# Performance work log

Hardware: AMD Instinct MI355X
Metric: run time of the kernel (lower is better)

Reference implementation:

```python
import jax, jax.numpy as jnp
import numpy as np


def _conv(x, w, stride, padding):
    # x: NCHW, w: OIHW
    return jax.lax.conv_general_dilated(
        x, w,
        window_strides=(stride, stride),
        padding=[(padding, padding), (padding, padding)],
        dimension_numbers=("NCHW", "OIHW", "NCHW"),
    )


def setup_inputs() -> dict:
    key = jax.random.key(0)
    ks = jax.random.split(key, 7)
    N, C_in, H0, W0 = 64, 128, 56, 56
    C_out = 256
    x = jax.random.normal(ks[0], (N, C_in, H0, W0), dtype=jnp.float32)
    w1 = jax.random.normal(ks[1], (C_out, C_in, 3, 3), dtype=jnp.float32) * 0.05
    b1 = jax.random.normal(ks[2], (C_out,), dtype=jnp.float32) * 0.05
    w2 = jax.random.normal(ks[3], (C_out, C_out, 3, 3), dtype=jnp.float32) * 0.05
    b2 = jax.random.normal(ks[4], (C_out,), dtype=jnp.float32) * 0.05
    wds = jax.random.normal(ks[5], (C_out, C_in, 1, 1), dtype=jnp.float32) * 0.05
    bds = jax.random.normal(ks[6], (C_out,), dtype=jnp.float32) * 0.05
    return {"x": x, "w1": w1, "b1": b1, "w2": w2, "b2": b2, "wds": wds, "bds": bds}


def reference(x, w1, b1, w2, b2, wds, bds):
    stride = 2
    # conv1 (BN folded) + bias + ReLU -> act: (N, C_out, H1, W1)
    act = jax.nn.relu(_conv(x, w1, stride, 1) + b1[None, :, None, None])
    # fused: conv2 3x3 (pad 1) + b2 + 1x1 strided downsample of x + bds, then ReLU
    main = _conv(act, w2, 1, 1) + b2[None, :, None, None]
    shortcut = _conv(x, wds, stride, 0) + bds[None, :, None, None]
    return jax.nn.relu(main + shortcut)
```

## Files before the change

kernel.cpp:

```cpp
#include <hip/hip_runtime.h>
#include <hip/hip_bf16.h>

typedef short short8 __attribute__((ext_vector_type(8)));
typedef float floatx4 __attribute__((ext_vector_type(4)));
typedef __hip_bfloat16 bf16;

#define GLB(p) ((const __attribute__((address_space(1))) void*)(p))
#define LDSP(p) ((__attribute__((address_space(3))) void*)(p))

__device__ __forceinline__ void gload16(const bf16* g, char* l) {
    __builtin_amdgcn_global_load_lds(GLB(g), LDSP(l), 16, 0, 0);
}

#define XPAD_BYTES   (64u*58*58*128*2)
#define ACTPAD_BYTES (64u*30*30*256*2)
#define OFF_XPAD   0
#define OFF_ACTPAD (XPAD_BYTES)
#define OFF_W1T    (OFF_ACTPAD + ACTPAD_BYTES)
#define OFF_W2T    (OFF_W1T + 1152u*256*2)
#define OFF_WDST   (OFF_W2T + 2304u*256*2)

__global__ void wtrans_kernel(const float* __restrict__ w1, const float* __restrict__ w2,
                              const float* __restrict__ wds,
                              bf16* __restrict__ w1t, bf16* __restrict__ w2t,
                              bf16* __restrict__ wdst) {
    int i = blockIdx.x * 256 + threadIdx.x;
    if (i < 256 * 1152) {
        int oc = i / 1152, k = i % 1152, tap = k >> 7, ic = k & 127;
        w1t[i] = __float2bfloat16(w1[(oc * 128 + ic) * 9 + tap]);
    }
    if (i < 256 * 2304) {
        int oc = i / 2304, k = i % 2304, tap = k >> 8, ic = k & 255;
        w2t[i] = __float2bfloat16(w2[(oc * 256 + ic) * 9 + tap]);
    }
    if (i < 256 * 128) {
        wdst[i] = __float2bfloat16(wds[i]);
    }
}

__global__ void xpad_kernel(const float* __restrict__ x, bf16* __restrict__ xpad) {
    int bid = blockIdx.x;
    int n = bid / 56, h = bid % 56;
    __shared__ float tile[128 * 57];
    const float* src = x + ((size_t)n * 128) * 3136 + h * 56;
    for (int e = threadIdx.x; e < 128 * 56; e += 256) {
        int c = e / 56, w = e % 56;
        tile[c * 57 + w] = src[(size_t)c * 3136 + w];
    }
    __syncthreads();
    bf16* dst = xpad + ((size_t)(n * 58 + h + 1) * 58 + 1) * 128;
    for (int e = threadIdx.x; e < 56 * 16; e += 256) {
        int w = e / 16, g = e % 16;
        union { bf16 b[8]; uint4 v; } o;
        #pragma unroll
        for (int j = 0; j < 8; ++j)
            o.b[j] = __float2bfloat16(tile[(g * 8 + j) * 57 + w]);
        *(uint4*)(dst + (size_t)w * 128 + g * 8) = o.v;
    }
}

__global__ __launch_bounds__(256) void conv1_kernel(
    const bf16* __restrict__ xpad, const bf16* __restrict__ w1t,
    const float* __restrict__ b1, bf16* __restrict__ actpad)
{
    __shared__ __align__(16) char lds[32768];
    const int t = threadIdx.x;
    const int oc0 = blockIdx.x * 128;
    const int m0  = blockIdx.y * 128;

    const int srow = t >> 3, sunit = t & 7;
    const int uo = ((sunit ^ (srow & 7)) << 3);

    size_t aeoff[4], weoff[4];
    #pragma unroll
    for (int i = 0; i < 4; ++i) {
        int r = srow + 32 * i;
        int m = m0 + r;
        int n = m / 784, pix = m % 784;
        int oh = pix / 28, ow = pix % 28;
        aeoff[i] = (size_t)((n * 58 + 2 * oh) * 58 + 2 * ow) * 128 + uo;
        weoff[i] = (size_t)(oc0 + r) * 1152 + uo;
    }
    const int ldsa0 = t * 16;
    const int ldsw0 = 16384 + t * 16;

    const int lane = t & 63, wid = t >> 6;
    const int wm = (wid >> 1) << 6, woc = (wid & 1) << 6;
    const int lrow = lane & 15, lhi = lane >> 4;
    int aoffs[4][2], woffs[4][2];
    #pragma unroll
    for (int f = 0; f < 4; ++f)
        #pragma unroll
        for (int h = 0; h < 2; ++h) {
            int ra = wm + f * 16 + lrow;
            aoffs[f][h] = ra * 128 + (((lhi + (h << 2)) ^ (ra & 7)) << 4);
            int rw = woc + f * 16 + lrow;
            woffs[f][h] = 16384 + rw * 128 + (((lhi + (h << 2)) ^ (rw & 7)) << 4);
        }

    floatx4 acc[4][4];
    #pragma unroll
    for (int a = 0; a < 4; ++a)
        #pragma unroll
        for (int b = 0; b < 4; ++b) acc[a][b] = (floatx4){0.f, 0.f, 0.f, 0.f};

    for (int s = 0; s < 18; ++s) {
        int tap = s >> 1, chunk = s & 1;
        int kh = tap / 3, kw = tap % 3;
        size_t aoff = (size_t)(kh * 58 + kw) * 128 + chunk * 64;
        size_t woff = (size_t)s * 64;
        #pragma unroll
        for (int i = 0; i < 4; ++i) gload16(xpad + aeoff[i] + aoff, lds + ldsa0 + i * 4096);
        #pragma unroll
        for (int i = 0; i < 4; ++i) gload16(w1t + weoff[i] + woff, lds + ldsw0 + i * 4096);
        __syncthreads();
        #pragma unroll
        for (int h = 0; h < 2; ++h) {
            short8 af[4], wf[4];
            #pragma unroll
            for (int f = 0; f < 4; ++f) af[f] = *(const short8*)(lds + aoffs[f][h]);
            #pragma unroll
            for (int f = 0; f < 4; ++f) wf[f] = *(const short8*)(lds + woffs[f][h]);
            #pragma unroll
            for (int fm = 0; fm < 4; ++fm)
                #pragma unroll
                for (int fo = 0; fo < 4; ++fo)
                    acc[fm][fo] = __builtin_amdgcn_mfma_f32_16x16x32_bf16(af[fm], wf[fo], acc[fm][fo], 0, 0, 0);
        }
        __syncthreads();
    }

    #pragma unroll
    for (int fm = 0; fm < 4; ++fm) {
        #pragma unroll
        for (int rg = 0; rg < 4; ++rg) {
            int m = m0 + wm + fm * 16 + (lhi << 2) + rg;
            int n = m / 784, pix = m % 784;
            int oh = pix / 28, ow = pix % 28;
            bf16* dst = actpad + ((size_t)(n * 30 + oh + 1) * 30 + (ow + 1)) * 256;
            #pragma unroll
            for (int fo = 0; fo < 4; ++fo) {
                int oc = oc0 + woc + fo * 16 + lrow;
                float v = acc[fm][fo][rg] + b1[oc];
                dst[oc] = __float2bfloat16(fmaxf(v, 0.0f));
            }
        }
    }
}

__global__ __launch_bounds__(256) void conv2_kernel(
    const bf16* __restrict__ actpad, const bf16* __restrict__ xpad,
    const bf16* __restrict__ w2t, const bf16* __restrict__ wdst,
    const float* __restrict__ b2, const float* __restrict__ bds,
    float* __restrict__ out)
{
    __shared__ __align__(16) char lds[32768];
    const int t = threadIdx.x;
    const int oc0 = blockIdx.x * 128;
    const int m0  = blockIdx.y * 128;

    const int srow = t >> 3, sunit = t & 7;
    const int uo = ((sunit ^ (srow & 7)) << 3);

    size_t aeoff[4], weoff[4];
    int pk[4];
    #pragma unroll
    for (int i = 0; i < 4; ++i) {
        int r = srow + 32 * i;
        int m = m0 + r;
        int n = m / 784, pix = m % 784;
        int oh = pix / 28, ow = pix % 28;
        pk[i] = (n << 10) | (oh << 5) | ow;
        aeoff[i] = (size_t)((n * 30 + oh) * 30 + ow) * 256 + uo;
        weoff[i] = (size_t)(oc0 + r) * 2304 + uo;
    }
    const int ldsa0 = t * 16;
    const int ldsw0 = 16384 + t * 16;

    const int lane = t & 63, wid = t >> 6;
    const int wm = (wid >> 1) << 6, woc = (wid & 1) << 6;
    const int lrow = lane & 15, lhi = lane >> 4;
    int aoffs[4][2], woffs[4][2];
    #pragma unroll
    for (int f = 0; f < 4; ++f)
        #pragma unroll
        for (int h = 0; h < 2; ++h) {
            int ra = wm + f * 16 + lrow;
            aoffs[f][h] = ra * 128 + (((lhi + (h << 2)) ^ (ra & 7)) << 4);
            int rw = woc + f * 16 + lrow;
            woffs[f][h] = 16384 + rw * 128 + (((lhi + (h << 2)) ^ (rw & 7)) << 4);
        }

    floatx4 acc[4][4];
    #pragma unroll
    for (int a = 0; a < 4; ++a)
        #pragma unroll
        for (int b = 0; b < 4; ++b) acc[a][b] = (floatx4){0.f, 0.f, 0.f, 0.f};

    for (int s = 0; s < 38; ++s) {
        if (s < 36) {
            int tap = s >> 2, chunk = s & 3;
            int kh = tap / 3, kw = tap % 3;
            size_t aoff = (size_t)(kh * 30 + kw) * 256 + chunk * 64;
            size_t woff = (size_t)s * 64;
            #pragma unroll
            for (int i = 0; i < 4; ++i) gload16(actpad + aeoff[i] + aoff, lds + ldsa0 + i * 4096);
            #pragma unroll
            for (int i = 0; i < 4; ++i) gload16(w2t + weoff[i] + woff, lds + ldsw0 + i * 4096);
        } else {
            int chunk = s - 36;
            #pragma unroll
            for (int i = 0; i < 4; ++i) {
                int n = pk[i] >> 10, oh = (pk[i] >> 5) & 31, ow = pk[i] & 31;
                gload16(xpad + (size_t)((n * 58 + 2 * oh + 1) * 58 + (2 * ow + 1)) * 128 + uo + chunk * 64,
                        lds + ldsa0 + i * 4096);
                int r = srow + 32 * i;
                gload16(wdst + (size_t)(oc0 + r) * 128 + uo + chunk * 64, lds + ldsw0 + i * 4096);
            }
        }
        __syncthreads();
        #pragma unroll
        for (int h = 0; h < 2; ++h) {
            short8 af[4], wf[4];
            #pragma unroll
            for (int f = 0; f < 4; ++f) af[f] = *(const short8*)(lds + aoffs[f][h]);
            #pragma unroll
            for (int f = 0; f < 4; ++f) wf[f] = *(const short8*)(lds + woffs[f][h]);
            #pragma unroll
            for (int fm = 0; fm < 4; ++fm)
                #pragma unroll
                for (int fo = 0; fo < 4; ++fo)
                    acc[fm][fo] = __builtin_amdgcn_mfma_f32_16x16x32_bf16(wf[fo], af[fm], acc[fm][fo], 0, 0, 0);
        }
        __syncthreads();
    }

    #pragma unroll
    for (int fm = 0; fm < 4; ++fm) {
        int mcol = m0 + wm + fm * 16 + lrow;
        int n = mcol / 784, pix = mcol % 784;
        float* obase = out + (size_t)n * 200704 + pix;
        #pragma unroll
        for (int fo = 0; fo < 4; ++fo) {
            int ocb = oc0 + woc + fo * 16 + (lhi << 2);
            #pragma unroll
            for (int rg = 0; rg < 4; ++rg) {
                int oc = ocb + rg;
                float v = acc[fm][fo][rg] + b2[oc] + bds[oc];
                obase[(size_t)oc * 784] = fmaxf(v, 0.0f);
            }
        }
    }
}

extern "C" void kernel_launch(void* const* d_in, const int* in_sizes, int n_in,
                              void* d_out, int out_size, void* d_ws, size_t ws_size,
                              hipStream_t stream) {
    const float* x   = (const float*)d_in[0];
    const float* w1  = (const float*)d_in[1];
    const float* b1  = (const float*)d_in[2];
    const float* w2  = (const float*)d_in[3];
    const float* b2  = (const float*)d_in[4];
    const float* wds = (const float*)d_in[5];
    const float* bds = (const float*)d_in[6];
    float* out = (float*)d_out;

    char* ws = (char*)d_ws;
    bf16* xpad   = (bf16*)(ws + OFF_XPAD);
    bf16* actpad = (bf16*)(ws + OFF_ACTPAD);
    bf16* w1t    = (bf16*)(ws + OFF_W1T);
    bf16* w2t    = (bf16*)(ws + OFF_W2T);
    bf16* wdst   = (bf16*)(ws + OFF_WDST);

    hipMemsetAsync(xpad, 0, XPAD_BYTES, stream);
    hipMemsetAsync(actpad, 0, ACTPAD_BYTES, stream);

    wtrans_kernel<<<2304, 256, 0, stream>>>(w1, w2, wds, w1t, w2t, wdst);
    xpad_kernel<<<64 * 56, 256, 0, stream>>>(x, xpad);
    conv1_kernel<<<dim3(2, 392), 256, 0, stream>>>(xpad, w1t, b1, actpad);
    conv2_kernel<<<dim3(2, 392), 256, 0, stream>>>(actpad, xpad, w2t, wdst, b2, bds, out);
}
```

Measured before the change: 343.7 us.

## Rewrite conv kernels as 256x256-tile multi-stage pipelined GEMMs and zero only halos

Both implicit-GEMM conv kernels now use 512-thread blocks. Each block computes a 256-pixel by 256-channel tile with 8x4 MFMA fragments per wave. Global-to-LDS loads go through a 4-slot, 128KB LDS ring kept three stages ahead, with explicit vmcnt waits, barriers and raised wave priority around the MFMA blocks. The full-buffer memsets of the padded activation buffers are replaced by a kernel that zeroes only the halo rows and columns, cutting tens of MB of writes. The trade-offs are that the grid shrinks to 196 blocks, so some CUs sit idle, occupancy is limited by the large LDS footprint, and the old XOR swizzle on LDS rows is dropped, which risks bank conflicts.

```diff
diff --git a/kernel.cpp b/kernel.cpp
--- a/kernel.cpp
+++ b/kernel.cpp
@@ -11,6 +11,10 @@
 __device__ __forceinline__ void gload16(const bf16* g, char* l) {
     __builtin_amdgcn_global_load_lds(GLB(g), LDSP(l), 16, 0, 0);
 }
+
+#define VMCNT(n) asm volatile("s_waitcnt vmcnt(" #n ")" ::: "memory")
+#define LGKM0()  asm volatile("s_waitcnt lgkmcnt(0)" ::: "memory")
+#define BAR()    __builtin_amdgcn_s_barrier()
 
 #define XPAD_BYTES   (64u*58*58*128*2)
 #define ACTPAD_BYTES (64u*30*30*256*2)
@@ -38,6 +42,35 @@
     }
 }
 
+__global__ void halo_zero_kernel(bf16* __restrict__ xpad, bf16* __restrict__ actpad) {
+    int i = blockIdx.x * 256 + threadIdx.x;
+    uint4 z; z.x = z.y = z.z = z.w = 0;
+    const int n0 = 64 * 2 * 58 * 16;
+    const int n1 = n0 + 64 * 56 * 2 * 16;
+    const int n2 = n1 + 64 * 2 * 30 * 32;
+    const int n3 = n2 + 64 * 28 * 2 * 32;
+    if (i < n0) {
+        int g = i & 15, w = (i >> 4) % 58, q = (i >> 4) / 58;
+        int n = q >> 1, h = (q & 1) ? 57 : 0;
+        *(uint4*)(xpad + ((size_t)((n * 58 + h) * 58 + w)) * 128 + g * 8) = z;
+    } else if (i < n1) {
+        int j = i - n0;
+        int g = j & 15, q = j >> 4;
+        int w = (q & 1) ? 57 : 0, h = (q >> 1) % 56 + 1, n = (q >> 1) / 56;
+        *(uint4*)(xpad + ((size_t)((n * 58 + h) * 58 + w)) * 128 + g * 8) = z;
+    } else if (i < n2) {
+        int j = i - n1;
+        int g = j & 31, w = (j >> 5) % 30, q = (j >> 5) / 30;
+        int n = q >> 1, h = (q & 1) ? 29 : 0;
+        *(uint4*)(actpad + ((size_t)((n * 30 + h) * 30 + w)) * 256 + g * 8) = z;
+    } else if (i < n3) {
+        int j = i - n2;
+        int g = j & 31, q = j >> 5;
+        int w = (q & 1) ? 29 : 0, h = (q >> 1) % 28 + 1, n = (q >> 1) / 28;
+        *(uint4*)(actpad + ((size_t)((n * 30 + h) * 30 + w)) * 256 + g * 8) = z;
+    }
+}
+
 __global__ void xpad_kernel(const float* __restrict__ x, bf16* __restrict__ xpad) {
     int bid = blockIdx.x;
     int n = bid / 56, h = bid % 56;
@@ -59,88 +92,112 @@
     }
 }
 
-__global__ __launch_bounds__(256) void conv1_kernel(
+__global__ __launch_bounds__(512, 2) void conv1_kernel(
     const bf16* __restrict__ xpad, const bf16* __restrict__ w1t,
     const float* __restrict__ b1, bf16* __restrict__ actpad)
 {
-    __shared__ __align__(16) char lds[32768];
+    __shared__ __align__(16) char lds[131072];
     const int t = threadIdx.x;
-    const int oc0 = blockIdx.x * 128;
-    const int m0  = blockIdx.y * 128;
-
-    const int srow = t >> 3, sunit = t & 7;
-    const int uo = ((sunit ^ (srow & 7)) << 3);
-
-    size_t aeoff[4], weoff[4];
-    #pragma unroll
-    for (int i = 0; i < 4; ++i) {
-        int r = srow + 32 * i;
-        int m = m0 + r;
-        int n = m / 784, pix = m % 784;
-        int oh = pix / 28, ow = pix % 28;
-        aeoff[i] = (size_t)((n * 58 + 2 * oh) * 58 + 2 * ow) * 128 + uo;
-        weoff[i] = (size_t)(oc0 + r) * 1152 + uo;
-    }
-    const int ldsa0 = t * 16;
-    const int ldsw0 = 16384 + t * 16;
+    const int m0 = blockIdx.x * 256;
+
+    const int unit = t & 3, srow = t >> 2;
+    int xb[2], wb[2];
+    #pragma unroll
+    for (int r = 0; r < 2; ++r) {
+        int m = m0 + r * 128 + srow;
+        int n = m / 784, pix = m % 784, oh = pix / 28, ow = pix % 28;
+        xb[r] = ((n * 58 + 2 * oh) * 58 + 2 * ow) * 128 + unit * 8;
+        wb[r] = (r * 128 + srow) * 1152 + unit * 8;
+    }
+    char* const ldsA = lds + t * 16;
+    char* const ldsB = lds + 16384 + t * 16;
+
+    auto STAGE_A = [&](int kt, int slot) {
+        int tap = kt >> 2, chunk = kt & 3;
+        int kh = (tap * 11) >> 5, kw = tap - kh * 3;
+        int toff = (kh * 58 + kw) * 128 + chunk * 32;
+        gload16(xpad + xb[0] + toff, ldsA + slot * 32768);
+        gload16(xpad + xb[1] + toff, ldsA + slot * 32768 + 8192);
+    };
+    auto STAGE_B = [&](int kt, int slot) {
+        gload16(w1t + wb[0] + kt * 32, ldsB + slot * 32768);
+        gload16(w1t + wb[1] + kt * 32, ldsB + slot * 32768 + 8192);
+    };
 
     const int lane = t & 63, wid = t >> 6;
-    const int wm = (wid >> 1) << 6, woc = (wid & 1) << 6;
-    const int lrow = lane & 15, lhi = lane >> 4;
-    int aoffs[4][2], woffs[4][2];
-    #pragma unroll
-    for (int f = 0; f < 4; ++f)
-        #pragma unroll
-        for (int h = 0; h < 2; ++h) {
-            int ra = wm + f * 16 + lrow;
-            aoffs[f][h] = ra * 128 + (((lhi + (h << 2)) ^ (ra & 7)) << 4);
-            int rw = woc + f * 16 + lrow;
-            woffs[f][h] = 16384 + rw * 128 + (((lhi + (h << 2)) ^ (rw & 7)) << 4);
-        }
-
-    floatx4 acc[4][4];
-    #pragma unroll
-    for (int a = 0; a < 4; ++a)
+    const int wm = (wid >> 2) << 7, woc = (wid & 3) << 6;
+    const int lr = lane & 15, kg = lane >> 4;
+    int aoff[8], boff[4];
+    #pragma unroll
+    for (int f = 0; f < 8; ++f) aoff[f] = (wm + f * 16 + lr) * 64 + kg * 16;
+    #pragma unroll
+    for (int g = 0; g < 4; ++g) boff[g] = 16384 + (woc + g * 16 + lr) * 64 + kg * 16;
+
+    floatx4 acc[8][4];
+    #pragma unroll
+    for (int a = 0; a < 8; ++a)
         #pragma unroll
         for (int b = 0; b < 4; ++b) acc[a][b] = (floatx4){0.f, 0.f, 0.f, 0.f};
 
-    for (int s = 0; s < 18; ++s) {
-        int tap = s >> 1, chunk = s & 1;
-        int kh = tap / 3, kw = tap % 3;
-        size_t aoff = (size_t)(kh * 58 + kw) * 128 + chunk * 64;
-        size_t woff = (size_t)s * 64;
-        #pragma unroll
-        for (int i = 0; i < 4; ++i) gload16(xpad + aeoff[i] + aoff, lds + ldsa0 + i * 4096);
-        #pragma unroll
-        for (int i = 0; i < 4; ++i) gload16(w1t + weoff[i] + woff, lds + ldsw0 + i * 4096);
-        __syncthreads();
-        #pragma unroll
-        for (int h = 0; h < 2; ++h) {
-            short8 af[4], wf[4];
-            #pragma unroll
-            for (int f = 0; f < 4; ++f) af[f] = *(const short8*)(lds + aoffs[f][h]);
-            #pragma unroll
-            for (int f = 0; f < 4; ++f) wf[f] = *(const short8*)(lds + woffs[f][h]);
-            #pragma unroll
-            for (int fm = 0; fm < 4; ++fm)
+    STAGE_A(0, 0); STAGE_B(0, 0);
+    STAGE_A(1, 1); STAGE_B(1, 1);
+    STAGE_A(2, 2); STAGE_B(2, 2);
+    VMCNT(8); BAR();
+
+    #pragma unroll 4
+    for (int kt = 0; kt < 36; ++kt) {
+        const int cs = kt & 3;
+        const char* base = lds + (cs << 15);
+        short8 wfr[4];
+        #pragma unroll
+        for (int g = 0; g < 4; ++g) wfr[g] = *(const short8*)(base + boff[g]);
+        {
+            short8 afr[4];
+            #pragma unroll
+            for (int f = 0; f < 4; ++f) afr[f] = *(const short8*)(base + aoff[f]);
+            if (kt + 3 < 36) STAGE_A(kt + 3, (kt + 3) & 3);
+            BAR(); LGKM0();
+            __builtin_amdgcn_s_setprio(1);
+            #pragma unroll
+            for (int f = 0; f < 4; ++f)
                 #pragma unroll
                 for (int fo = 0; fo < 4; ++fo)
-                    acc[fm][fo] = __builtin_amdgcn_mfma_f32_16x16x32_bf16(af[fm], wf[fo], acc[fm][fo], 0, 0, 0);
-        }
-        __syncthreads();
-    }
-
-    #pragma unroll
-    for (int fm = 0; fm < 4; ++fm) {
+                    acc[f][fo] = __builtin_amdgcn_mfma_f32_16x16x32_bf16(afr[f], wfr[fo], acc[f][fo], 0, 0, 0);
+            __builtin_amdgcn_s_setprio(0);
+            BAR();
+        }
+        {
+            short8 afr[4];
+            #pragma unroll
+            for (int f = 0; f < 4; ++f) afr[f] = *(const short8*)(base + aoff[4 + f]);
+            if (kt + 3 < 36) STAGE_B(kt + 3, (kt + 3) & 3);
+            BAR(); LGKM0();
+            __builtin_amdgcn_s_setprio(1);
+            #pragma unroll
+            for (int f = 0; f < 4; ++f)
+                #pragma unroll
+                for (int fo = 0; fo < 4; ++fo)
+                    acc[4 + f][fo] = __builtin_amdgcn_mfma_f32_16x16x32_bf16(afr[f], wfr[fo], acc[4 + f][fo], 0, 0, 0);
+            __builtin_amdgcn_s_setprio(0);
+            int rem = 35 - kt;
+            if (rem >= 3) { VMCNT(8); }
+            else if (rem == 2) { VMCNT(4); }
+            else if (rem == 1) { VMCNT(0); }
+            BAR();
+        }
+    }
+
+    #pragma unroll
+    for (int fm = 0; fm < 8; ++fm) {
         #pragma unroll
         for (int rg = 0; rg < 4; ++rg) {
-            int m = m0 + wm + fm * 16 + (lhi << 2) + rg;
+            int m = m0 + wm + fm * 16 + (kg << 2) + rg;
             int n = m / 784, pix = m % 784;
             int oh = pix / 28, ow = pix % 28;
             bf16* dst = actpad + ((size_t)(n * 30 + oh + 1) * 30 + (ow + 1)) * 256;
             #pragma unroll
             for (int fo = 0; fo < 4; ++fo) {
-                int oc = oc0 + woc + fo * 16 + lrow;
+                int oc = woc + fo * 16 + lr;
                 float v = acc[fm][fo][rg] + b1[oc];
                 dst[oc] = __float2bfloat16(fmaxf(v, 0.0f));
             }
@@ -148,101 +205,125 @@
     }
 }
 
-__global__ __launch_bounds__(256) void conv2_kernel(
+__global__ __launch_bounds__(512, 2) void conv2_kernel(
     const bf16* __restrict__ actpad, const bf16* __restrict__ xpad,
     const bf16* __restrict__ w2t, const bf16* __restrict__ wdst,
     const float* __restrict__ b2, const float* __restrict__ bds,
     float* __restrict__ out)
 {
-    __shared__ __align__(16) char lds[32768];
+    __shared__ __align__(16) char lds[131072];
     const int t = threadIdx.x;
-    const int oc0 = blockIdx.x * 128;
-    const int m0  = blockIdx.y * 128;
-
-    const int srow = t >> 3, sunit = t & 7;
-    const int uo = ((sunit ^ (srow & 7)) << 3);
-
-    size_t aeoff[4], weoff[4];
-    int pk[4];
-    #pragma unroll
-    for (int i = 0; i < 4; ++i) {
-        int r = srow + 32 * i;
-        int m = m0 + r;
-        int n = m / 784, pix = m % 784;
-        int oh = pix / 28, ow = pix % 28;
-        pk[i] = (n << 10) | (oh << 5) | ow;
-        aeoff[i] = (size_t)((n * 30 + oh) * 30 + ow) * 256 + uo;
-        weoff[i] = (size_t)(oc0 + r) * 2304 + uo;
-    }
-    const int ldsa0 = t * 16;
-    const int ldsw0 = 16384 + t * 16;
+    const int m0 = blockIdx.x * 256;
+
+    const int unit = t & 3, srow = t >> 2;
+    int ab[2], xb[2], wb[2], db[2];
+    #pragma unroll
+    for (int r = 0; r < 2; ++r) {
+        int m = m0 + r * 128 + srow;
+        int n = m / 784, pix = m % 784, oh = pix / 28, ow = pix % 28;
+        ab[r] = ((n * 30 + oh) * 30 + ow) * 256 + unit * 8;
+        xb[r] = ((n * 58 + 2 * oh + 1) * 58 + (2 * ow + 1)) * 128 + unit * 8;
+        wb[r] = (r * 128 + srow) * 2304 + unit * 8;
+        db[r] = (r * 128 + srow) * 128 + unit * 8;
+    }
+    char* const ldsA = lds + t * 16;
+    char* const ldsB = lds + 16384 + t * 16;
+
+    auto STAGE_A = [&](int kt, int slot) {
+        if (kt < 72) {
+            int tap = kt >> 3, chunk = kt & 7;
+            int kh = (tap * 11) >> 5, kw = tap - kh * 3;
+            int toff = (kh * 30 + kw) * 256 + chunk * 32;
+            gload16(actpad + ab[0] + toff, ldsA + slot * 32768);
+            gload16(actpad + ab[1] + toff, ldsA + slot * 32768 + 8192);
+        } else {
+            int chunk = kt - 72;
+            gload16(xpad + xb[0] + chunk * 32, ldsA + slot * 32768);
+            gload16(xpad + xb[1] + chunk * 32, ldsA + slot * 32768 + 8192);
+        }
+    };
+    auto STAGE_B = [&](int kt, int slot) {
+        if (kt < 72) {
+            gload16(w2t + wb[0] + kt * 32, ldsB + slot * 32768);
+            gload16(w2t + wb[1] + kt * 32, ldsB + slot * 32768 + 8192);
+        } else {
+            int chunk = kt - 72;
+            gload16(wdst + db[0] + chunk * 32, ldsB + slot * 32768);
+            gload16(wdst + db[1] + chunk * 32, ldsB + slot * 32768 + 8192);
+        }
+    };
 
     const int lane = t & 63, wid = t >> 6;
-    const int wm = (wid >> 1) << 6, woc = (wid & 1) << 6;
-    const int lrow = lane & 15, lhi = lane >> 4;
-    int aoffs[4][2], woffs[4][2];
-    #pragma unroll
-    for (int f = 0; f < 4; ++f)
-        #pragma unroll
-        for (int h = 0; h < 2; ++h) {
-            int ra = wm + f * 16 + lrow;
-            aoffs[f][h] = ra * 128 + (((lhi + (h << 2)) ^ (ra & 7)) << 4);
-            int rw = woc + f * 16 + lrow;
-            woffs[f][h] = 16384 + rw * 128 + (((lhi + (h << 2)) ^ (rw & 7)) << 4);
-        }
-
-    floatx4 acc[4][4];
-    #pragma unroll
-    for (int a = 0; a < 4; ++a)
+    const int wm = (wid >> 2) << 7, woc = (wid & 3) << 6;
+    const int lr = lane & 15, kg = lane >> 4;
+    int aoff[8], boff[4];
+    #pragma unroll
+    for (int f = 0; f < 8; ++f) aoff[f] = (wm + f * 16 + lr) * 64 + kg * 16;
+    #pragma unroll
+    for (int g = 0; g < 4; ++g) boff[g] = 16384 + (woc + g * 16 + lr) * 64 + kg * 16;
+
+    floatx4 acc[8][4];
+    #pragma unroll
+    for (int a = 0; a < 8; ++a)
         #pragma unroll
         for (int b = 0; b < 4; ++b) acc[a][b] = (floatx4){0.f, 0.f, 0.f, 0.f};
 
-    for (int s = 0; s < 38; ++s) {
-        if (s < 36) {
-            int tap = s >> 2, chunk = s & 3;
-            int kh = tap / 3, kw = tap % 3;
-            size_t aoff = (size_t)(kh * 30 + kw) * 256 + chunk * 64;
-            size_t woff = (size_t)s * 64;
-            #pragma unroll
-            for (int i = 0; i < 4; ++i) gload16(actpad + aeoff[i] + aoff, lds + ldsa0 + i * 4096);
-            #pragma unroll
-            for (int i = 0; i < 4; ++i) gload16(w2t + weoff[i] + woff, lds + ldsw0 + i * 4096);
-        } else {
-            int chunk = s - 36;
-            #pragma unroll
-            for (int i = 0; i < 4; ++i) {
-                int n = pk[i] >> 10, oh = (pk[i] >> 5) & 31, ow = pk[i] & 31;
-                gload16(xpad + (size_t)((n * 58 + 2 * oh + 1) * 58 + (2 * ow + 1)) * 128 + uo + chunk * 64,
-                        lds + ldsa0 + i * 4096);
-                int r = srow + 32 * i;
-                gload16(wdst + (size_t)(oc0 + r) * 128 + uo + chunk * 64, lds + ldsw0 + i * 4096);
-            }
-        }
-        __syncthreads();
-        #pragma unroll
-        for (int h = 0; h < 2; ++h) {
-            short8 af[4], wf[4];
-            #pragma unroll
-            for (int f = 0; f < 4; ++f) af[f] = *(const short8*)(lds + aoffs[f][h]);
-            #pragma unroll
-            for (int f = 0; f < 4; ++f) wf[f] = *(const short8*)(lds + woffs[f][h]);
-            #pragma unroll
-            for (int fm = 0; fm < 4; ++fm)
+    STAGE_A(0, 0); STAGE_B(0, 0);
+    STAGE_A(1, 1); STAGE_B(1, 1);
+    STAGE_A(2, 2); STAGE_B(2, 2);
+    VMCNT(8); BAR();
+
+    #pragma unroll 4
+    for (int kt = 0; kt < 76; ++kt) {
+        const int cs = kt & 3;
+        const char* base = lds + (cs << 15);
+        short8 wfr[4];
+        #pragma unroll
+        for (int g = 0; g < 4; ++g) wfr[g] = *(const short8*)(base + boff[g]);
+        {
+            short8 afr[4];
+            #pragma unroll
+            for (int f = 0; f < 4; ++f) afr[f] = *(const short8*)(base + aoff[f]);
+            if (kt + 3 < 76) STAGE_A(kt + 3, (kt + 3) & 3);
+            BAR(); LGKM0();
+            __builtin_amdgcn_s_setprio(1);
+            #pragma unroll
+            for (int f = 0; f < 4; ++f)
                 #pragma unroll
                 for (int fo = 0; fo < 4; ++fo)
-                    acc[fm][fo] = __builtin_amdgcn_mfma_f32_16x16x32_bf16(wf[fo], af[fm], acc[fm][fo], 0, 0, 0);
-        }
-        __syncthreads();
-    }
-
-    #pragma unroll
-    for (int fm = 0; fm < 4; ++fm) {
-        int mcol = m0 + wm + fm * 16 + lrow;
+                    acc[f][fo] = __builtin_amdgcn_mfma_f32_16x16x32_bf16(wfr[fo], afr[f], acc[f][fo], 0, 0, 0);
+            __builtin_amdgcn_s_setprio(0);
+            BAR();
+        }
+        {
+            short8 afr[4];
+            #pragma unroll
+            for (int f = 0; f < 4; ++f) afr[f] = *(const short8*)(base + aoff[4 + f]);
+            if (kt + 3 < 76) STAGE_B(kt + 3, (kt + 3) & 3);
+            BAR(); LGKM0();
+            __builtin_amdgcn_s_setprio(1);
+            #pragma unroll
+            for (int f = 0; f < 4; ++f)
+                #pragma unroll
+                for (int fo = 0; fo < 4; ++fo)
+                    acc[4 + f][fo] = __builtin_amdgcn_mfma_f32_16x16x32_bf16(wfr[fo], afr[f], acc[4 + f][fo], 0, 0, 0);
+            __builtin_amdgcn_s_setprio(0);
+            int rem = 75 - kt;
+            if (rem >= 3) { VMCNT(8); }
+            else if (rem == 2) { VMCNT(4); }
+            else if (rem == 1) { VMCNT(0); }
+            BAR();
+        }
+    }
+
+    #pragma unroll
+    for (int fm = 0; fm < 8; ++fm) {
+        int mcol = m0 + wm + fm * 16 + lr;
         int n = mcol / 784, pix = mcol % 784;
         float* obase = out + (size_t)n * 200704 + pix;
         #pragma unroll
         for (int fo = 0; fo < 4; ++fo) {
-            int ocb = oc0 + woc + fo * 16 + (lhi << 2);
+            int ocb = woc + fo * 16 + (kg << 2);
             #pragma unroll
             for (int rg = 0; rg < 4; ++rg) {
                 int oc = ocb + rg;
@@ -272,11 +353,9 @@
     bf16* w2t    = (bf16*)(ws + OFF_W2T);
     bf16* wdst   = (bf16*)(ws + OFF_WDST);
 
-    hipMemsetAsync(xpad, 0, XPAD_BYTES, stream);
-    hipMemsetAsync(actpad, 0, ACTPAD_BYTES, stream);
-
+    halo_zero_kernel<<<1840, 256, 0, stream>>>(xpad, actpad);
     wtrans_kernel<<<2304, 256, 0, stream>>>(w1, w2, wds, w1t, w2t, wdst);
     xpad_kernel<<<64 * 56, 256, 0, stream>>>(x, xpad);
-    conv1_kernel<<<dim3(2, 392), 256, 0, stream>>>(xpad, w1t, b1, actpad);
-    conv2_kernel<<<dim3(2, 392), 256, 0, stream>>>(actpad, xpad, w2t, wdst, b2, bds, out);
-}
+    conv1_kernel<<<196, 512, 0, stream>>>(xpad, w1t, b1, actpad);
+    conv2_kernel<<<196, 512, 0, stream>>>(actpad, xpad, w2t, wdst, b2, bds, out);
+}
```

After: 321.6 us. 1.07x faster.
